# Performance work log

Measured on AMD Instinct MI355X. Metric: run time of the kernel, lower is better.

## Reference

```python
import jax, jax.numpy as jnp
import numpy as np

N = 40000        # total gene nodes
E = 640000       # edges
F_IN = 128       # num_features
H = 128          # hidden_dim
SUB = 400        # genes per cell
EPS = 1e-5


def _bn(x, g, b):
    # BatchNorm1d, training-mode batch statistics (biased variance), deterministic
    m = x.mean(axis=0)
    v = x.var(axis=0)
    return (x - m) * jax.lax.rsqrt(v + EPS) * g + b


def _gcn_conv(x, W, b, src, dst):
    # PyG GCNConv: h = X W; add self-loops; symmetric deg^{-1/2} normalization;
    # scatter-add messages from src into dst; then add bias.
    h = x @ W                                   # [N, H]
    loop = jnp.arange(N)
    s = jnp.concatenate([src, loop])            # [E+N]
    d = jnp.concatenate([dst, loop])
    deg = jax.ops.segment_sum(jnp.ones(s.shape[0], h.dtype), d, num_segments=N)
    dis = jnp.where(deg > 0, deg ** -0.5, 0.0)  # deg_inv_sqrt
    norm = dis[s] * dis[d]                      # [E+N]
    out = jax.ops.segment_sum(h[s] * norm[:, None], d, num_segments=N)
    return out + b


def setup_inputs() -> dict:
    key = jax.random.key(0)
    ks = jax.random.split(key, 16)
    sc = lambda fan: 1.0 / np.sqrt(fan)
    inp = {
        "x": jax.random.normal(ks[0], (N, F_IN), jnp.float32),
        "edge_index": jax.random.randint(ks[1], (2, E), 0, N, jnp.int64),
        "conv1_w": jax.random.normal(ks[2], (F_IN, H), jnp.float32) * sc(F_IN),
        "conv1_b": jnp.zeros((H,), jnp.float32),
        "bn1_g": jnp.ones((H,), jnp.float32),
        "bn1_b": jnp.zeros((H,), jnp.float32),
        "conv2_w": jax.random.normal(ks[3], (H, H), jnp.float32) * sc(H),
        "conv2_b": jnp.zeros((H,), jnp.float32),
        "bn2_g": jnp.ones((H,), jnp.float32),
        "bn2_b": jnp.zeros((H,), jnp.float32),
        "att_w1": jax.random.normal(ks[4], (H, H // 2), jnp.float32) * sc(H),
        "att_b1": jnp.zeros((H // 2,), jnp.float32),
        "att_w2": jax.random.normal(ks[5], (H // 2, 1), jnp.float32) * sc(H // 2),
        "att_b2": jnp.zeros((1,), jnp.float32),
        "fc_w": jax.random.normal(ks[6], (H, H), jnp.float32) * sc(H),
        "fc_b": jnp.zeros((H,), jnp.float32),
        "bne_g": jnp.ones((H,), jnp.float32),
        "bne_b": jnp.zeros((H,), jnp.float32),
        "bot_w": jax.random.normal(ks[7], (H, 32), jnp.float32) * sc(H),
        "bot_b": jnp.zeros((32,), jnp.float32),
        "bnb_g": jnp.ones((32,), jnp.float32),
        "bnb_b": jnp.zeros((32,), jnp.float32),
    }
    return inp


def reference(x, edge_index, conv1_w, conv1_b, bn1_g, bn1_b,
              conv2_w, conv2_b, bn2_g, bn2_b,
              att_w1, att_b1, att_w2, att_b2,
              fc_w, fc_b, bne_g, bne_b,
              bot_w, bot_b, bnb_g, bnb_b):
    src, dst = edge_index[0], edge_index[1]
    # embed: two GCNConv + BN + ReLU (dropout omitted: deterministic reference)
    h = jax.nn.relu(_bn(_gcn_conv(x, conv1_w, conv1_b, src, dst), bn1_g, bn1_b))
    emb = jax.nn.relu(_bn(_gcn_conv(h, conv2_w, conv2_b, src, dst), bn2_g, bn2_b))
    # attention pooling over genes within each cell
    num_cells = N // SUB
    xr = emb.reshape(num_cells, SUB, H)                      # [C, S, H]
    scores = jnp.tanh(xr @ att_w1 + att_b1) @ att_w2 + att_b2  # [C, S, 1]
    w = jax.nn.softmax(scores, axis=1)
    pooled = jnp.sum(xr * w, axis=1)                          # [C, H]
    # dense head
    y = jax.nn.relu(_bn(pooled @ fc_w + fc_b, bne_g, bne_b))
    y = jax.nn.relu(_bn(y @ bot_w + bot_b, bnb_g, bnb_b))     # [C, 32]
    return (y, emb)
```

## Files before the change

kernel.cpp:

```cpp
#include <hip/hip_runtime.h>
#include <math.h>

typedef unsigned int u32;
typedef unsigned short u16;
typedef __attribute__((ext_vector_type(8))) short bf16x8;
typedef __attribute__((ext_vector_type(4))) float f32x4;

#define NN   40000
#define EE   640000
#define SUBG 400
#define CELLS 100
#define BNEPS 1e-5f
#define GB    2048
#define GEMMB 625
#define DEGB  1024
#define FILLB 1024

__device__ __forceinline__ u32 bf16pair(float a, float b) {
    u32 ua = __float_as_uint(a), ub = __float_as_uint(b);
    ua += 0x7fffu + ((ua >> 16) & 1u);
    ub += 0x7fffu + ((ub >> 16) & 1u);
    return (ua >> 16) | (ub & 0xffff0000u);
}
__device__ __forceinline__ float bflo(u32 u) { return __uint_as_float(u << 16); }
__device__ __forceinline__ float bfhi(u32 u) { return __uint_as_float(u & 0xffff0000u); }

__global__ void k_init(int* deg_cursor, const float* W1, u32* Wt1,
                       const float* W2, u32* Wt2, const float* wa, u32* Wta,
                       float* hstats) {
    int i = blockIdx.x * 256 + threadIdx.x;
    if (i < 2 * NN) { deg_cursor[i] = 0; return; }
    i -= 2 * NN;
    if (i < 16384) {
        const float* W = (i < 8192) ? W1 : W2;
        u32* Wt = (i < 8192) ? Wt1 : Wt2;
        int j = i & 8191;
        int n = j >> 6, k2 = (j & 63) * 2;
        Wt[n * 64 + (j & 63)] = bf16pair(W[k2 * 128 + n], W[(k2 + 1) * 128 + n]);
        return;
    }
    i -= 16384;
    if (i < 4096) {
        int n = i >> 6, k2 = (i & 63) * 2;
        Wta[n * 64 + (i & 63)] = bf16pair(wa[k2 * 64 + n], wa[(k2 + 1) * 64 + n]);
        return;
    }
    i -= 4096;
    if (i < 320) hstats[i] = 0.f;
}

__global__ void k_degcount(const int* __restrict__ dst, int* __restrict__ deg) {
    int i = blockIdx.x * blockDim.x + threadIdx.x;
    int stride = DEGB * 256;
    for (; i < EE; i += stride) atomicAdd(&deg[dst[i]], 1);
}

__global__ __launch_bounds__(1024)
void k_scan(const int* __restrict__ deg, int* __restrict__ rowstart,
            float* __restrict__ dis) {
    __shared__ int ps[1024];
    int t = threadIdx.x;
    const int4* d4 = (const int4*)deg;
    int sum = 0;
#pragma unroll
    for (int j = 0; j < 10; ++j) {
        int i4 = t * 10 + j;
        if (i4 < 10000) {
            int4 v = d4[i4];
            sum += v.x + v.y + v.z + v.w;
        }
    }
    ps[t] = sum;
    __syncthreads();
    for (int off = 1; off < 1024; off <<= 1) {
        int add = (t >= off) ? ps[t - off] : 0;
        __syncthreads();
        ps[t] += add;
        __syncthreads();
    }
    int run = ps[t] - sum;
#pragma unroll
    for (int j = 0; j < 10; ++j) {
        int i4 = t * 10 + j;
        if (i4 < 10000) {
            int4 v = d4[i4];
            int4 r;
            r.x = run;
            r.y = run + v.x;
            r.z = r.y + v.y;
            r.w = r.z + v.z;
            run = r.w + v.w;
            *(int4*)&rowstart[i4 * 4] = r;
            float4 dv;
            dv.x = rsqrtf((float)(v.x + 1));
            dv.y = rsqrtf((float)(v.y + 1));
            dv.z = rsqrtf((float)(v.z + 1));
            dv.w = rsqrtf((float)(v.w + 1));
            *(float4*)&dis[i4 * 4] = dv;
        }
    }
    if (t == 0) rowstart[NN] = EE;
}

__global__ __launch_bounds__(256)
void k_fillgemm(const int* __restrict__ src, const int* __restrict__ dst,
                const int* __restrict__ rowstart, int* __restrict__ cursor,
                u16* __restrict__ csr16,
                const float* __restrict__ X, const u32* __restrict__ Wt,
                u32* __restrict__ Yb, const float* __restrict__ dis) {
    int bid = blockIdx.x;
    int t = threadIdx.x;
    if (bid < FILLB) {
        int i = bid * 256 + t;
        int stride = FILLB * 256;
        for (; i < EE; i += stride) {
            int d = dst[i];
            int slot = rowstart[d] + atomicAdd(&cursor[d], 1);
            csr16[slot] = (u16)src[i];
        }
        return;
    }
    int l = t & 63, wv = t >> 6;
    int rowbase = (bid - FILLB) * 64 + wv * 16;
    int ml = l & 15, kg = l >> 4;

    f32x4 acc[8];
#pragma unroll
    for (int nt = 0; nt < 8; ++nt) acc[nt] = (f32x4){0.f, 0.f, 0.f, 0.f};
    const float* xr = X + (long)(rowbase + ml) * 128;
#pragma unroll
    for (int kk = 0; kk < 4; ++kk) {
        int k0 = kk * 32 + kg * 8;
        float4 xa = *(const float4*)&xr[k0];
        float4 xb = *(const float4*)&xr[k0 + 4];
        union { u32 u[4]; bf16x8 v; } af;
        af.u[0] = bf16pair(xa.x, xa.y);
        af.u[1] = bf16pair(xa.z, xa.w);
        af.u[2] = bf16pair(xb.x, xb.y);
        af.u[3] = bf16pair(xb.z, xb.w);
#pragma unroll
        for (int nt = 0; nt < 8; ++nt) {
            bf16x8 b = *(const bf16x8*)&Wt[(nt * 16 + ml) * 64 + (k0 >> 1)];
            acc[nt] = __builtin_amdgcn_mfma_f32_16x16x32_bf16(af.v, b, acc[nt], 0, 0, 0);
        }
    }
#pragma unroll
    for (int r = 0; r < 4; ++r) {
        int m = rowbase + kg * 4 + r;
        float dd = dis[m];
        long obase = (long)m * 64;
#pragma unroll
        for (int nt = 0; nt < 8; ++nt) {
            float v = acc[nt][r] * dd;
            float v2 = __shfl_xor(v, 1);
            if ((l & 1) == 0)
                Yb[obase + nt * 8 + (ml >> 1)] = bf16pair(v, v2);
        }
    }
}

__global__ __launch_bounds__(256)
void k_gemm_bf16(const u32* __restrict__ Xb, const u32* __restrict__ Wt,
                 u32* __restrict__ Yb, const float* __restrict__ ss,
                 const float* __restrict__ dis) {
    int t = threadIdx.x;
    int l = t & 63, wv = t >> 6;
    int rowbase = blockIdx.x * 64 + wv * 16;
    int ml = l & 15, kg = l >> 4;

    f32x4 acc[8];
#pragma unroll
    for (int nt = 0; nt < 8; ++nt) acc[nt] = (f32x4){0.f, 0.f, 0.f, 0.f};
    const u32* xr = Xb + (long)(rowbase + ml) * 64;
#pragma unroll
    for (int kk = 0; kk < 4; ++kk) {
        int k0 = kk * 32 + kg * 8;
        uint4 xw = *(const uint4*)&xr[k0 >> 1];
        float f0 = bflo(xw.x), f1 = bfhi(xw.x), f2 = bflo(xw.y), f3 = bfhi(xw.y);
        float f4 = bflo(xw.z), f5 = bfhi(xw.z), f6 = bflo(xw.w), f7 = bfhi(xw.w);
        float4 sca = *(const float4*)&ss[k0];
        float4 sha = *(const float4*)&ss[128 + k0];
        float4 scb = *(const float4*)&ss[k0 + 4];
        float4 shb = *(const float4*)&ss[128 + k0 + 4];
        f0 = fmaxf(fmaf(f0, sca.x, sha.x), 0.f);
        f1 = fmaxf(fmaf(f1, sca.y, sha.y), 0.f);
        f2 = fmaxf(fmaf(f2, sca.z, sha.z), 0.f);
        f3 = fmaxf(fmaf(f3, sca.w, sha.w), 0.f);
        f4 = fmaxf(fmaf(f4, scb.x, shb.x), 0.f);
        f5 = fmaxf(fmaf(f5, scb.y, shb.y), 0.f);
        f6 = fmaxf(fmaf(f6, scb.z, shb.z), 0.f);
        f7 = fmaxf(fmaf(f7, scb.w, shb.w), 0.f);
        union { u32 u[4]; bf16x8 v; } af;
        af.u[0] = bf16pair(f0, f1);
        af.u[1] = bf16pair(f2, f3);
        af.u[2] = bf16pair(f4, f5);
        af.u[3] = bf16pair(f6, f7);
#pragma unroll
        for (int nt = 0; nt < 8; ++nt) {
            bf16x8 b = *(const bf16x8*)&Wt[(nt * 16 + ml) * 64 + (k0 >> 1)];
            acc[nt] = __builtin_amdgcn_mfma_f32_16x16x32_bf16(af.v, b, acc[nt], 0, 0, 0);
        }
    }
#pragma unroll
    for (int r = 0; r < 4; ++r) {
        int m = rowbase + kg * 4 + r;
        float dd = dis[m];
        long obase = (long)m * 64;
#pragma unroll
        for (int nt = 0; nt < 8; ++nt) {
            float v = acc[nt][r] * dd;
            float v2 = __shfl_xor(v, 1);
            if ((l & 1) == 0)
                Yb[obase + nt * 8 + (ml >> 1)] = bf16pair(v, v2);
        }
    }
}

__global__ __launch_bounds__(256)
void k_gather_stats(const uint4* __restrict__ Hb, const int* __restrict__ rowstart,
                    const u16* __restrict__ csr16, const float* __restrict__ dis,
                    const float* __restrict__ bias, u32* __restrict__ F1b,
                    float* __restrict__ part) {
    __shared__ float ls[1024], lq[1024];
    int t = threadIdx.x;
    int lane = t & 63, wv = t >> 6;
    int gw = blockIdx.x * 4 + wv;
    int g = lane >> 4, p = lane & 15;
    int c0 = p * 8 + g * 2;
    float2 bb = *(const float2*)&bias[c0];
    float s0 = 0.f, s1 = 0.f, q0 = 0.f, q1 = 0.f;

    for (int node = gw; node < NN; node += GB * 4) {
        float a0 = 0.f, a1 = 0.f, a2 = 0.f, a3 = 0.f, a4 = 0.f, a5 = 0.f, a6 = 0.f, a7 = 0.f;
        if (g == 0) {
            uint4 h = Hb[node * 16 + p];
            a0 = bflo(h.x); a1 = bfhi(h.x);
            a2 = bflo(h.y); a3 = bfhi(h.y);
            a4 = bflo(h.z); a5 = bfhi(h.z);
            a6 = bflo(h.w); a7 = bfhi(h.w);
        }
        int e1 = rowstart[node + 1];
        int e = rowstart[node] + g;
        for (; e + 4 < e1; e += 8) {
            int sA = csr16[e];
            int sB = csr16[e + 4];
            uint4 h0 = Hb[sA * 16 + p];
            uint4 h1 = Hb[sB * 16 + p];
            a0 += bflo(h0.x); a1 += bfhi(h0.x);
            a2 += bflo(h0.y); a3 += bfhi(h0.y);
            a4 += bflo(h0.z); a5 += bfhi(h0.z);
            a6 += bflo(h0.w); a7 += bfhi(h0.w);
            a0 += bflo(h1.x); a1 += bfhi(h1.x);
            a2 += bflo(h1.y); a3 += bfhi(h1.y);
            a4 += bflo(h1.z); a5 += bfhi(h1.z);
            a6 += bflo(h1.w); a7 += bfhi(h1.w);
        }
        if (e < e1) {
            int sA = csr16[e];
            uint4 h0 = Hb[sA * 16 + p];
            a0 += bflo(h0.x); a1 += bfhi(h0.x);
            a2 += bflo(h0.y); a3 += bfhi(h0.y);
            a4 += bflo(h0.z); a5 += bfhi(h0.z);
            a6 += bflo(h0.w); a7 += bfhi(h0.w);
        }
#pragma unroll
        for (int m = 16; m <= 32; m <<= 1) {
            a0 += __shfl_xor(a0, m); a1 += __shfl_xor(a1, m);
            a2 += __shfl_xor(a2, m); a3 += __shfl_xor(a3, m);
            a4 += __shfl_xor(a4, m); a5 += __shfl_xor(a5, m);
            a6 += __shfl_xor(a6, m); a7 += __shfl_xor(a7, m);
        }
        float dd = dis[node];
        float x = (g == 0) ? a0 : (g == 1) ? a2 : (g == 2) ? a4 : a6;
        float y = (g == 0) ? a1 : (g == 1) ? a3 : (g == 2) ? a5 : a7;
        x = fmaf(x, dd, bb.x);
        y = fmaf(y, dd, bb.y);
        u32 pw = bf16pair(x, y);
        F1b[node * 64 + (c0 >> 1)] = pw;
        float rx = bflo(pw), ry = bfhi(pw);
        s0 += rx; s1 += ry; q0 += rx * rx; q1 += ry * ry;
    }
    ls[wv * 128 + c0] = s0; ls[wv * 128 + c0 + 1] = s1;
    lq[wv * 128 + c0] = q0; lq[wv * 128 + c0 + 1] = q1;
    __syncthreads();
    if (t < 128) {
        float S = ls[t] + ls[128 + t] + ls[256 + t] + ls[384 + t];
        float Q = lq[t] + lq[128 + t] + lq[256 + t] + lq[384 + t];
        part[blockIdx.x * 256 + t] = S;
        part[blockIdx.x * 256 + 128 + t] = Q;
    }
}

__global__ __launch_bounds__(256)
void k_bnfinalw(const float* __restrict__ part, const float* __restrict__ g,
                const float* __restrict__ b, float* __restrict__ ss) {
    __shared__ float rs[256], rq[256];
    int c = blockIdx.x, t = threadIdx.x;
    float s = 0.f, q = 0.f;
    for (int i = t; i < GB; i += 256) {
        s += part[i * 256 + c];
        q += part[i * 256 + 128 + c];
    }
    rs[t] = s; rq[t] = q;
    __syncthreads();
    for (int off = 128; off > 0; off >>= 1) {
        if (t < off) { rs[t] += rs[t + off]; rq[t] += rq[t + off]; }
        __syncthreads();
    }
    if (t == 0) {
        float mean = rs[0] * (1.0f / NN);
        float var  = rq[0] * (1.0f / NN) - mean * mean;
        float sc = g[c] * rsqrtf(var + BNEPS);
        ss[c] = sc;
        ss[128 + c] = b[c] - mean * sc;
    }
}

__global__ __launch_bounds__(256)
void k_scoremb(const u32* __restrict__ F1b, const float* __restrict__ ss,
               float* __restrict__ emb,
               const u32* __restrict__ Wta, const float* __restrict__ b1,
               const float* __restrict__ w2, const float* __restrict__ b2,
               float* __restrict__ scores) {
    int t = threadIdx.x;
    int l = t & 63, wv = t >> 6;
    int rowbase = blockIdx.x * 64 + wv * 16;
    int ml = l & 15, kg = l >> 4;

    f32x4 acc[4];
#pragma unroll
    for (int nt = 0; nt < 4; ++nt) acc[nt] = (f32x4){0.f, 0.f, 0.f, 0.f};
    const u32* xr = F1b + (long)(rowbase + ml) * 64;
    float* er = emb + (long)(rowbase + ml) * 128;
#pragma unroll
    for (int kk = 0; kk < 4; ++kk) {
        int k0 = kk * 32 + kg * 8;
        uint4 xw = *(const uint4*)&xr[k0 >> 1];
        float f0 = bflo(xw.x), f1 = bfhi(xw.x), f2 = bflo(xw.y), f3 = bfhi(xw.y);
        float f4 = bflo(xw.z), f5 = bfhi(xw.z), f6 = bflo(xw.w), f7 = bfhi(xw.w);
        float4 sca = *(const float4*)&ss[k0];
        float4 sha = *(const float4*)&ss[128 + k0];
        float4 scb = *(const float4*)&ss[k0 + 4];
        float4 shb = *(const float4*)&ss[128 + k0 + 4];
        f0 = fmaxf(fmaf(f0, sca.x, sha.x), 0.f);
        f1 = fmaxf(fmaf(f1, sca.y, sha.y), 0.f);
        f2 = fmaxf(fmaf(f2, sca.z, sha.z), 0.f);
        f3 = fmaxf(fmaf(f3, sca.w, sha.w), 0.f);
        f4 = fmaxf(fmaf(f4, scb.x, shb.x), 0.f);
        f5 = fmaxf(fmaf(f5, scb.y, shb.y), 0.f);
        f6 = fmaxf(fmaf(f6, scb.z, shb.z), 0.f);
        f7 = fmaxf(fmaf(f7, scb.w, shb.w), 0.f);
        float4 e0 = { f0, f1, f2, f3 };
        float4 e1 = { f4, f5, f6, f7 };
        *(float4*)&er[k0] = e0;
        *(float4*)&er[k0 + 4] = e1;
        union { u32 u[4]; bf16x8 v; } af;
        af.u[0] = bf16pair(f0, f1);
        af.u[1] = bf16pair(f2, f3);
        af.u[2] = bf16pair(f4, f5);
        af.u[3] = bf16pair(f6, f7);
#pragma unroll
        for (int nt = 0; nt < 4; ++nt) {
            bf16x8 b = *(const bf16x8*)&Wta[(nt * 16 + ml) * 64 + (k0 >> 1)];
            acc[nt] = __builtin_amdgcn_mfma_f32_16x16x32_bf16(af.v, b, acc[nt], 0, 0, 0);
        }
    }
    float b1v[4], w2v[4];
#pragma unroll
    for (int nt = 0; nt < 4; ++nt) {
        b1v[nt] = b1[nt * 16 + ml];
        w2v[nt] = w2[nt * 16 + ml];
    }
    float b2v = b2[0];
#pragma unroll
    for (int r = 0; r < 4; ++r) {
        float s = tanhf(acc[0][r] + b1v[0]) * w2v[0]
                + tanhf(acc[1][r] + b1v[1]) * w2v[1]
                + tanhf(acc[2][r] + b1v[2]) * w2v[2]
                + tanhf(acc[3][r] + b1v[3]) * w2v[3];
        s += __shfl_xor(s, 1);
        s += __shfl_xor(s, 2);
        s += __shfl_xor(s, 4);
        s += __shfl_xor(s, 8);
        if (ml == 0) scores[rowbase + kg * 4 + r] = s + b2v;
    }
}

__global__ __launch_bounds__(256)
void k_pool4(const u32* __restrict__ F1b, const float* __restrict__ ss,
             const float* __restrict__ scores, float* __restrict__ pp) {
    __shared__ float sl[SUBG];
    __shared__ float red[256];
    __shared__ float rbuf[512];
    int b = blockIdx.x;
    int c = b >> 2, q = b & 3;
    int t = threadIdx.x;
    int base = c * SUBG;

    float lmax = -1e30f;
    for (int i = t; i < SUBG; i += 256) {
        float v = scores[base + i];
        sl[i] = v;
        lmax = fmaxf(lmax, v);
    }
    red[t] = lmax;
    __syncthreads();
    for (int off = 128; off > 0; off >>= 1) {
        if (t < off) red[t] = fmaxf(red[t], red[t + off]);
        __syncthreads();
    }
    float mx = red[0];
    __syncthreads();
    float lsum = 0.f;
    for (int i = t; i < SUBG; i += 256) {
        float e = __expf(sl[i] - mx);
        sl[i] = e;
        lsum += e;
    }
    red[t] = lsum;
    __syncthreads();
    for (int off = 128; off > 0; off >>= 1) {
        if (t < off) red[t] += red[t + off];
        __syncthreads();
    }
    float inv = 1.0f / red[0];
    __syncthreads();

    int cc = t & 63, gp = t >> 6;
    float2 scv = *(const float2*)&ss[2 * cc];
    float2 shv = *(const float2*)&ss[128 + 2 * cc];
    int g0 = q * 100 + gp * 25;
    float a0 = 0.f, a1 = 0.f;
#pragma unroll 5
    for (int j = 0; j < 25; ++j) {
        int gg = g0 + j;
        u32 v = F1b[(long)(base + gg) * 64 + cc];
        float w = sl[gg] * inv;
        float x0 = fmaxf(fmaf(bflo(v), scv.x, shv.x), 0.f);
        float x1 = fmaxf(fmaf(bfhi(v), scv.y, shv.y), 0.f);
        a0 += w * x0;
        a1 += w * x1;
    }
    rbuf[gp * 128 + 2 * cc] = a0;
    rbuf[gp * 128 + 2 * cc + 1] = a1;
    __syncthreads();
    if (t < 128)
        pp[b * 128 + t] = rbuf[t] + rbuf[128 + t] + rbuf[256 + t] + rbuf[384 + t];
}

__global__ __launch_bounds__(128)
void k_head1r(const float* __restrict__ pp, const float* __restrict__ fc_w,
              const float* __restrict__ fc_b, float* __restrict__ y1pre,
              float* __restrict__ hstats) {
    __shared__ float pr[128];
    int c = blockIdx.x, t = threadIdx.x;
    pr[t] = pp[(c * 4 + 0) * 128 + t] + pp[(c * 4 + 1) * 128 + t]
          + pp[(c * 4 + 2) * 128 + t] + pp[(c * 4 + 3) * 128 + t];
    __syncthreads();
    float a1 = fc_b[t];
#pragma unroll 4
    for (int k = 0; k < 128; ++k) a1 = fmaf(pr[k], fc_w[k * 128 + t], a1);
    y1pre[c * 128 + t] = a1;
    atomicAdd(&hstats[t], a1);
    atomicAdd(&hstats[128 + t], a1 * a1);
}

__global__ __launch_bounds__(128)
void k_head2s(const float* __restrict__ y1pre, const float* __restrict__ hstats,
              const float* __restrict__ bne_g, const float* __restrict__ bne_b,
              const float* __restrict__ bot_w, const float* __restrict__ bot_b,
              float* __restrict__ y2pre, float* __restrict__ hstats2) {
    __shared__ float row[128];
    int c = blockIdx.x, t = threadIdx.x;
    float s = hstats[t], q = hstats[128 + t];
    float mean = s * 0.01f, var = q * 0.01f - mean * mean;
    float scv = bne_g[t] * rsqrtf(var + BNEPS);
    float shv = bne_b[t] - mean * scv;
    row[t] = fmaxf(fmaf(y1pre[c * 128 + t], scv, shv), 0.f);
    __syncthreads();
    if (t < 32) {
        float a2 = bot_b[t];
#pragma unroll 4
        for (int k = 0; k < 128; ++k) a2 = fmaf(row[k], bot_w[k * 32 + t], a2);
        y2pre[c * 32 + t] = a2;
        atomicAdd(&hstats2[t], a2);
        atomicAdd(&hstats2[32 + t], a2 * a2);
    }
}

__global__ __launch_bounds__(256)
void k_out(const float* __restrict__ y2pre, const float* __restrict__ hstats2,
           const float* __restrict__ bnb_g, const float* __restrict__ bnb_b,
           float* __restrict__ y_out) {
    __shared__ float scv[32], shv[32];
    int t = threadIdx.x;
    if (t < 32) {
        float s = hstats2[t], q = hstats2[32 + t];
        float mean = s * 0.01f, var = q * 0.01f - mean * mean;
        float v = bnb_g[t] * rsqrtf(var + BNEPS);
        scv[t] = v; shv[t] = bnb_b[t] - mean * v;
    }
    __syncthreads();
    for (int i = t; i < CELLS * 32; i += 256)
        y_out[i] = fmaxf(fmaf(y2pre[i], scv[i & 31], shv[i & 31]), 0.f);
}

extern "C" void kernel_launch(void* const* d_in, const int* in_sizes, int n_in,
                              void* d_out, int out_size, void* d_ws, size_t ws_size,
                              hipStream_t stream) {
    const float* x        = (const float*)d_in[0];
    const int*   ei       = (const int*)d_in[1];
    const float* conv1_w  = (const float*)d_in[2];
    const float* conv1_b  = (const float*)d_in[3];
    const float* bn1_g    = (const float*)d_in[4];
    const float* bn1_b    = (const float*)d_in[5];
    const float* conv2_w  = (const float*)d_in[6];
    const float* conv2_b  = (const float*)d_in[7];
    const float* bn2_g    = (const float*)d_in[8];
    const float* bn2_b    = (const float*)d_in[9];
    const float* att_w1   = (const float*)d_in[10];
    const float* att_b1   = (const float*)d_in[11];
    const float* att_w2   = (const float*)d_in[12];
    const float* att_b2   = (const float*)d_in[13];
    const float* fc_w     = (const float*)d_in[14];
    const float* fc_b     = (const float*)d_in[15];
    const float* bne_g    = (const float*)d_in[16];
    const float* bne_b    = (const float*)d_in[17];
    const float* bot_w    = (const float*)d_in[18];
    const float* bot_b    = (const float*)d_in[19];
    const float* bnb_g    = (const float*)d_in[20];
    const float* bnb_b    = (const float*)d_in[21];

    const int* src = ei;
    const int* dst = ei + EE;

    float* y_out   = (float*)d_out;
    float* emb_out = y_out + CELLS * 32;

    float* ws = (float*)d_ws;
    u32*   Hb     = (u32*)ws;
    u32*   F1b    = Hb + (long)NN * 64;
    float* dis    = (float*)(F1b + (long)NN * 64);
    float* part   = dis + NN;
    float* ss     = part + GB * 256;
    float* hstats = ss + 256;
    float* y1pre  = hstats + 320;
    float* y2pre  = y1pre + CELLS * 128;
    float* scores = y2pre + CELLS * 32;
    float* pp     = scores + NN;
    u32*   Wt1    = (u32*)(pp + 400 * 128);
    u32*   Wt2    = Wt1 + 8192;
    u32*   Wta    = Wt2 + 8192;
    int*   deg    = (int*)(Wta + 4096);
    int*   cursor = deg + NN;
    int*   rowstart = cursor + NN;
    u16*   csr16  = (u16*)(rowstart + NN + 1);

    k_init<<<394, 256, 0, stream>>>(deg, conv1_w, Wt1, conv2_w, Wt2, att_w1, Wta, hstats);
    k_degcount<<<DEGB, 256, 0, stream>>>(dst, deg);
    k_scan<<<1, 1024, 0, stream>>>(deg, rowstart, dis);
    k_fillgemm<<<FILLB + GEMMB, 256, 0, stream>>>(src, dst, rowstart, cursor, csr16,
                                                  x, Wt1, Hb, dis);
    k_gather_stats<<<GB, 256, 0, stream>>>((const uint4*)Hb, rowstart, csr16, dis,
                                           conv1_b, F1b, part);
    k_bnfinalw<<<128, 256, 0, stream>>>(part, bn1_g, bn1_b, ss);
    k_gemm_bf16<<<GEMMB, 256, 0, stream>>>(F1b, Wt2, Hb, ss, dis);
    k_gather_stats<<<GB, 256, 0, stream>>>((const uint4*)Hb, rowstart, csr16, dis,
                                           conv2_b, F1b, part);
    k_bnfinalw<<<128, 256, 0, stream>>>(part, bn2_g, bn2_b, ss);
    k_scoremb<<<GEMMB, 256, 0, stream>>>(F1b, ss, emb_out, Wta, att_b1, att_w2,
                                         att_b2, scores);
    k_pool4<<<4 * CELLS, 256, 0, stream>>>(F1b, ss, scores, pp);
    k_head1r<<<CELLS, 128, 0, stream>>>(pp, fc_w, fc_b, y1pre, hstats);
    k_head2s<<<CELLS, 128, 0, stream>>>(y1pre, hstats, bne_g, bne_b, bot_w, bot_b,
                                        y2pre, hstats + 256);
    k_out<<<1, 256, 0, stream>>>(y2pre, hstats + 256, bnb_g, bnb_b, y_out);
}
```

Before: 240.1 us.

## Fuse init with degree count, partition CSR fill by dst range, merge head kernels

Measured after the change: 327.9 us. 1.37x slower.

```diff
diff --git a/kernel.cpp b/kernel.cpp
--- a/kernel.cpp
+++ b/kernel.cpp
@@ -14,7 +14,7 @@
 #define GB    2048
 #define GEMMB 625
 #define DEGB  1024
-#define FILLB 1024
+#define FILLB 512
 
 __device__ __forceinline__ u32 bf16pair(float a, float b) {
     u32 ua = __float_as_uint(a), ub = __float_as_uint(b);
@@ -25,12 +25,20 @@
 __device__ __forceinline__ float bflo(u32 u) { return __uint_as_float(u << 16); }
 __device__ __forceinline__ float bfhi(u32 u) { return __uint_as_float(u & 0xffff0000u); }
 
-__global__ void k_init(int* deg_cursor, const float* W1, u32* Wt1,
-                       const float* W2, u32* Wt2, const float* wa, u32* Wta,
-                       float* hstats) {
-    int i = blockIdx.x * 256 + threadIdx.x;
-    if (i < 2 * NN) { deg_cursor[i] = 0; return; }
-    i -= 2 * NN;
+__global__ __launch_bounds__(256)
+void k_degW(const int* __restrict__ dst, int* __restrict__ deg,
+            const float* __restrict__ W1, u32* __restrict__ Wt1,
+            const float* __restrict__ W2, u32* __restrict__ Wt2,
+            const float* __restrict__ wa, u32* __restrict__ Wta) {
+    int bid = blockIdx.x;
+    int t = threadIdx.x;
+    if (bid < DEGB) {
+        int i = bid * 256 + t;
+        int stride = DEGB * 256;
+        for (; i < EE; i += stride) atomicAdd(&deg[dst[i]], 1);
+        return;
+    }
+    int i = (bid - DEGB) * 256 + t;
     if (i < 16384) {
         const float* W = (i < 8192) ? W1 : W2;
         u32* Wt = (i < 8192) ? Wt1 : Wt2;
@@ -43,16 +51,7 @@
     if (i < 4096) {
         int n = i >> 6, k2 = (i & 63) * 2;
         Wta[n * 64 + (i & 63)] = bf16pair(wa[k2 * 64 + n], wa[(k2 + 1) * 64 + n]);
-        return;
-    }
-    i -= 4096;
-    if (i < 320) hstats[i] = 0.f;
-}
-
-__global__ void k_degcount(const int* __restrict__ dst, int* __restrict__ deg) {
-    int i = blockIdx.x * blockDim.x + threadIdx.x;
-    int stride = DEGB * 256;
-    for (; i < EE; i += stride) atomicAdd(&deg[dst[i]], 1);
+    }
 }
 
 __global__ __launch_bounds__(1024)
@@ -111,12 +110,16 @@
     int bid = blockIdx.x;
     int t = threadIdx.x;
     if (bid < FILLB) {
-        int i = bid * 256 + t;
-        int stride = FILLB * 256;
+        int g = bid & 7;
+        int lo = g * (NN / 8), hi = lo + (NN / 8);
+        int i = (bid >> 3) * 256 + t;
+        int stride = (FILLB / 8) * 256;
         for (; i < EE; i += stride) {
             int d = dst[i];
-            int slot = rowstart[d] + atomicAdd(&cursor[d], 1);
-            csr16[slot] = (u16)src[i];
+            if (d >= lo && d < hi) {
+                int slot = rowstart[d] + atomicAdd(&cursor[d], 1);
+                csr16[slot] = (u16)src[i];
+            }
         }
         return;
     }
@@ -448,61 +451,81 @@
         pp[b * 128 + t] = rbuf[t] + rbuf[128 + t] + rbuf[256 + t] + rbuf[384 + t];
 }
 
-__global__ __launch_bounds__(128)
-void k_head1r(const float* __restrict__ pp, const float* __restrict__ fc_w,
-              const float* __restrict__ fc_b, float* __restrict__ y1pre,
-              float* __restrict__ hstats) {
-    __shared__ float pr[128];
-    int c = blockIdx.x, t = threadIdx.x;
-    pr[t] = pp[(c * 4 + 0) * 128 + t] + pp[(c * 4 + 1) * 128 + t]
-          + pp[(c * 4 + 2) * 128 + t] + pp[(c * 4 + 3) * 128 + t];
-    __syncthreads();
-    float a1 = fc_b[t];
+__global__ __launch_bounds__(512)
+void k_headall(const float* __restrict__ pp,
+               const float* __restrict__ fc_w, const float* __restrict__ fc_b,
+               const float* __restrict__ bne_g, const float* __restrict__ bne_b,
+               const float* __restrict__ bot_w, const float* __restrict__ bot_b,
+               const float* __restrict__ bnb_g, const float* __restrict__ bnb_b,
+               float* __restrict__ y_out) {
+    __shared__ float P[CELLS * 128];
+    __shared__ float Y1[CELLS * 128];
+    __shared__ float red[512], red2[512];
+    int t = threadIdx.x;
+
+    for (int i = t; i < CELLS * 128; i += 512) {
+        int c = i >> 7, col = i & 127;
+        int b = c * 512 + col;
+        P[i] = pp[b] + pp[b + 128] + pp[b + 256] + pp[b + 384];
+    }
+    __syncthreads();
+
+    int col = t & 127, cp = t >> 7;
+    float s = 0.f, q = 0.f;
+    float fb = fc_b[col];
+    for (int j = 0; j < 25; ++j) {
+        int c = cp + 4 * j;
+        float a = fb;
 #pragma unroll 4
-    for (int k = 0; k < 128; ++k) a1 = fmaf(pr[k], fc_w[k * 128 + t], a1);
-    y1pre[c * 128 + t] = a1;
-    atomicAdd(&hstats[t], a1);
-    atomicAdd(&hstats[128 + t], a1 * a1);
-}
-
-__global__ __launch_bounds__(128)
-void k_head2s(const float* __restrict__ y1pre, const float* __restrict__ hstats,
-              const float* __restrict__ bne_g, const float* __restrict__ bne_b,
-              const float* __restrict__ bot_w, const float* __restrict__ bot_b,
-              float* __restrict__ y2pre, float* __restrict__ hstats2) {
-    __shared__ float row[128];
-    int c = blockIdx.x, t = threadIdx.x;
-    float s = hstats[t], q = hstats[128 + t];
-    float mean = s * 0.01f, var = q * 0.01f - mean * mean;
-    float scv = bne_g[t] * rsqrtf(var + BNEPS);
-    float shv = bne_b[t] - mean * scv;
-    row[t] = fmaxf(fmaf(y1pre[c * 128 + t], scv, shv), 0.f);
+        for (int k = 0; k < 128; ++k) a = fmaf(P[c * 128 + k], fc_w[k * 128 + col], a);
+        Y1[c * 128 + col] = a;
+        s += a; q += a * a;
+    }
+    red[t] = s; red2[t] = q;
+    __syncthreads();
+    if (t < 128) {
+        float S = red[t] + red[t + 128] + red[t + 256] + red[t + 384];
+        float Q = red2[t] + red2[t + 128] + red2[t + 256] + red2[t + 384];
+        float mean = S * 0.01f, var = Q * 0.01f - mean * mean;
+        float sc = bne_g[t] * rsqrtf(var + BNEPS);
+        red[t] = sc; red2[t] = bne_b[t] - mean * sc;
+    }
+    __syncthreads();
+    float sc1 = red[col], sh1 = red2[col];
+    for (int j = 0; j < 25; ++j) {
+        int idx = (cp + 4 * j) * 128 + col;
+        Y1[idx] = fmaxf(fmaf(Y1[idx], sc1, sh1), 0.f);
+    }
+    __syncthreads();
+
+    int col2 = t & 31, g2 = t >> 5;
+    float s2 = 0.f, q2 = 0.f;
+    for (int j = 0; j < 7; ++j) {
+        int c = g2 + 16 * j;
+        if (c < CELLS) {
+            float a = bot_b[col2];
+#pragma unroll 4
+            for (int k = 0; k < 128; ++k) a = fmaf(Y1[c * 128 + k], bot_w[k * 32 + col2], a);
+            P[c * 32 + col2] = a;
+            s2 += a; q2 += a * a;
+        }
+    }
+    red[t] = s2; red2[t] = q2;
     __syncthreads();
     if (t < 32) {
-        float a2 = bot_b[t];
-#pragma unroll 4
-        for (int k = 0; k < 128; ++k) a2 = fmaf(row[k], bot_w[k * 32 + t], a2);
-        y2pre[c * 32 + t] = a2;
-        atomicAdd(&hstats2[t], a2);
-        atomicAdd(&hstats2[32 + t], a2 * a2);
-    }
-}
-
-__global__ __launch_bounds__(256)
-void k_out(const float* __restrict__ y2pre, const float* __restrict__ hstats2,
-           const float* __restrict__ bnb_g, const float* __restrict__ bnb_b,
-           float* __restrict__ y_out) {
-    __shared__ float scv[32], shv[32];
-    int t = threadIdx.x;
-    if (t < 32) {
-        float s = hstats2[t], q = hstats2[32 + t];
-        float mean = s * 0.01f, var = q * 0.01f - mean * mean;
+        float S = 0.f, Q = 0.f;
+        for (int u = 0; u < 16; ++u) { S += red[u * 32 + t]; Q += red2[u * 32 + t]; }
+        float mean = S * 0.01f, var = Q * 0.01f - mean * mean;
         float v = bnb_g[t] * rsqrtf(var + BNEPS);
-        scv[t] = v; shv[t] = bnb_b[t] - mean * v;
-    }
-    __syncthreads();
-    for (int i = t; i < CELLS * 32; i += 256)
-        y_out[i] = fmaxf(fmaf(y2pre[i], scv[i & 31], shv[i & 31]), 0.f);
+        red[t] = v; red2[t] = bnb_b[t] - mean * v;
+    }
+    __syncthreads();
+    float sc2 = red[col2], sh2 = red2[col2];
+    for (int j = 0; j < 7; ++j) {
+        int c = g2 + 16 * j;
+        if (c < CELLS)
+            y_out[c * 32 + col2] = fmaxf(fmaf(P[c * 32 + col2], sc2, sh2), 0.f);
+    }
 }
 
 extern "C" void kernel_launch(void* const* d_in, const int* in_sizes, int n_in,
@@ -543,10 +566,7 @@
     float* dis    = (float*)(F1b + (long)NN * 64);
     float* part   = dis + NN;
     float* ss     = part + GB * 256;
-    float* hstats = ss + 256;
-    float* y1pre  = hstats + 320;
-    float* y2pre  = y1pre + CELLS * 128;
-    float* scores = y2pre + CELLS * 32;
+    float* scores = ss + 256;
     float* pp     = scores + NN;
     u32*   Wt1    = (u32*)(pp + 400 * 128);
     u32*   Wt2    = Wt1 + 8192;
@@ -556,8 +576,9 @@
     int*   rowstart = cursor + NN;
     u16*   csr16  = (u16*)(rowstart + NN + 1);
 
-    k_init<<<394, 256, 0, stream>>>(deg, conv1_w, Wt1, conv2_w, Wt2, att_w1, Wta, hstats);
-    k_degcount<<<DEGB, 256, 0, stream>>>(dst, deg);
+    hipMemsetAsync(deg, 0, (size_t)2 * NN * sizeof(int), stream);
+    k_degW<<<DEGB + 80, 256, 0, stream>>>(dst, deg, conv1_w, Wt1, conv2_w, Wt2,
+                                          att_w1, Wta);
     k_scan<<<1, 1024, 0, stream>>>(deg, rowstart, dis);
     k_fillgemm<<<FILLB + GEMMB, 256, 0, stream>>>(src, dst, rowstart, cursor, csr16,
                                                   x, Wt1, Hb, dis);
@@ -571,8 +592,6 @@
     k_scoremb<<<GEMMB, 256, 0, stream>>>(F1b, ss, emb_out, Wta, att_b1, att_w2,
                                          att_b2, scores);
     k_pool4<<<4 * CELLS, 256, 0, stream>>>(F1b, ss, scores, pp);
-    k_head1r<<<CELLS, 128, 0, stream>>>(pp, fc_w, fc_b, y1pre, hstats);
-    k_head2s<<<CELLS, 128, 0, stream>>>(y1pre, hstats, bne_g, bne_b, bot_w, bot_b,
-                                        y2pre, hstats + 256);
-    k_out<<<1, 256, 0, stream>>>(y2pre, hstats + 256, bnb_g, bnb_b, y_out);
-}
+    k_headall<<<1, 512, 0, stream>>>(pp, fc_w, fc_b, bne_g, bne_b,
+                                     bot_w, bot_b, bnb_g, bnb_b, y_out);
+}
```
